# Kernel tuning notes

Hardware: AMD Instinct MI355X
Metric: run time of the kernel (lower is better)

The kernel has to match this reference:

```python
import math
import jax, jax.numpy as jnp
import numpy as np

N, L, H, E, K = 4, 768, 8, 64, 1  # batch, seq (L==S), heads, feat, num_sines


def setup_inputs() -> dict:
    key = jax.random.key(0)
    ks = jax.random.split(key, 8)
    queries = jax.random.normal(ks[0], (N, L, H, E), jnp.float32)
    keys = jax.random.normal(ks[1], (N, L, H, E), jnp.float32)
    values = jax.random.normal(ks[2], (N, L, H, E), jnp.float32)
    attn_mask_add = jnp.zeros((L, L), jnp.float32)
    key_lengths_add = jnp.zeros((N, L), jnp.float32)
    freqs = jax.random.normal(ks[3], (H, E, K), jnp.float32) - 4.0  # init shift
    offsets = jax.random.normal(ks[4], (H, E, K), jnp.float32)
    gains = jax.random.normal(ks[5], (H, E, K), jnp.float32)
    # gains.data /= sqrt(||gains||_{-1}) / 2
    gains = gains / (jnp.sqrt(jnp.linalg.norm(gains, axis=-1, keepdims=True)) / 2.0)
    gate = jax.random.normal(ks[6], (H, E), jnp.float32)
    return dict(queries=queries, keys=keys, values=values,
                attn_mask_add=attn_mask_add, key_lengths_add=key_lengths_add,
                freqs=freqs, offsets=offsets, gains=gains, gate=gate)


def reference(queries, keys, values, attn_mask_add, key_lengths_add,
              freqs, offsets, gains, gate):
    n, l, h, e = queries.shape
    softmax_temp = 1.0 / math.sqrt(e)
    positions = jnp.arange(l, dtype=queries.dtype)  # (L,)
    f = jax.nn.sigmoid(freqs)[None] / 2.0  # (1,H,E,K)
    phases_q = 2.0 * math.pi * f * positions[:, None, None, None] + offsets[None]
    phases_k = 2.0 * math.pi * f * positions[:, None, None, None]
    # interleave cos/sin along last dim -> (L,H,E,2K)
    omega_q = jnp.stack([jnp.cos(phases_q), jnp.sin(phases_q)], axis=-1).reshape(l, h, e, 2 * f.shape[-1])
    omega_k = jnp.stack([jnp.cos(phases_k), jnp.sin(phases_k)], axis=-1).reshape(l, h, e, 2 * f.shape[-1])
    g = jax.nn.softplus(gains)
    g2 = jnp.stack([g, g], axis=-1).reshape(h, e, 2 * f.shape[-1])  # (H,E,2K)
    # positional kernel P: (L,S,H,E)
    P = jnp.einsum('lhdk,hdk,shdk->lshd', omega_q, g2 ** 2, omega_k)
    P = (1.0 - gate) * P + gate  # gated
    QK = jnp.einsum('nlhd,lshd,nshd->nhls', queries, P, keys)
    QK = QK + attn_mask_add[None, None] + key_lengths_add[:, None, None, :]
    A = jax.nn.softmax(softmax_temp * QK, axis=-1)
    V = jnp.einsum('nhls,nshd->nlhd', A, values)
    return V
```

## Files before the change

kernel.cpp:

```cpp
#include <hip/hip_runtime.h>
#include <math.h>
#include <stdint.h>

#define NB 4
#define LQ 768
#define NH 8
#define NE 64
#define ND 192
#define TEMP 0.125f

typedef _Float16 f16;
typedef __attribute__((ext_vector_type(8))) _Float16 f16x8;
typedef __attribute__((ext_vector_type(4))) float f32x4;

__device__ __forceinline__ void stage16(f16* lds_base, const f16* g, int lane) {
#if __has_builtin(__builtin_amdgcn_global_load_lds)
    __builtin_amdgcn_global_load_lds(
        (const __attribute__((address_space(1))) uint32_t*)g,
        (__attribute__((address_space(3))) uint32_t*)lds_base, 16, 0, 0);
#else
    *(uint4*)((char*)lds_base + lane * 16) = *(const uint4*)g;
#endif
}

__global__ __launch_bounds__(256) void sinattn_prepvt(
    const float* __restrict__ Q, const float* __restrict__ K,
    const float* __restrict__ V,
    const float* __restrict__ freqs, const float* __restrict__ offsets,
    const float* __restrict__ gains, const float* __restrict__ gate,
    f16* __restrict__ Qf, f16* __restrict__ Kf, f16* __restrict__ Vt)
{
    if (blockIdx.x < 768) {
        int idx = blockIdx.x * 256 + threadIdx.x;
        int eg = idx & 7, e0 = eg << 3;
        int h  = (idx >> 3) & 7;
        int t  = idx >> 6;
        int l  = t % LQ;
        int n  = t / LQ;
        int nh = (n << 3) | h;
        int he = (h << 6) | e0;

        const float* qp = Q + (size_t)idx * 8;
        const float* kp = K + (size_t)idx * 8;
        float4 q0 = *(const float4*)qp, q1 = *(const float4*)(qp + 4);
        float4 k0 = *(const float4*)kp, k1 = *(const float4*)(kp + 4);
        float qv[8] = {q0.x,q0.y,q0.z,q0.w, q1.x,q1.y,q1.z,q1.w};
        float kv[8] = {k0.x,k0.y,k0.z,k0.w, k1.x,k1.y,k1.z,k1.w};

        float4 fA = *(const float4*)(freqs   + he), fB = *(const float4*)(freqs   + he + 4);
        float4 oA = *(const float4*)(offsets + he), oB = *(const float4*)(offsets + he + 4);
        float4 gA = *(const float4*)(gains   + he), gB = *(const float4*)(gains   + he + 4);
        float4 tA = *(const float4*)(gate    + he), tB = *(const float4*)(gate    + he + 4);
        float fv[8] = {fA.x,fA.y,fA.z,fA.w, fB.x,fB.y,fB.z,fB.w};
        float ov[8] = {oA.x,oA.y,oA.z,oA.w, oB.x,oB.y,oB.z,oB.w};
        float gv[8] = {gA.x,gA.y,gA.z,gA.w, gB.x,gB.y,gB.z,gB.w};
        float tv[8] = {tA.x,tA.y,tA.z,tA.w, tB.x,tB.y,tB.z,tB.w};

        f16x8 oq0, oq1, oq2, ok0, ok1, ok2;
        float lf = (float)l;
        #pragma unroll
        for (int j = 0; j < 8; ++j) {
            float f  = 0.5f / (1.0f + __expf(-fv[j]));
            float gn = gv[j];
            float sp = (gn > 15.0f) ? gn : __logf(1.0f + __expf(gn));
            float gt = tv[j];
            float a  = (1.0f - gt) * sp * sp;
            float fh = __uint_as_float(__float_as_uint(f) & 0xFFFFF000u);
            float fl = f - fh;
            float t0 = lf * fh;
            float tr = t0 - floorf(t0);
            tr = __builtin_fmaf(lf, fl, tr);
            float pk = 6.28318530717958647f * tr;
            float pq = pk + ov[j];
            float sq = __sinf(pq), cq = __cosf(pq);
            float sk = __sinf(pk), ck = __cosf(pk);
            oq0[j] = (f16)(qv[j] * a * cq);
            oq1[j] = (f16)(qv[j] * a * sq);
            oq2[j] = (f16)(qv[j] * gt);
            ok0[j] = (f16)(kv[j] * ck);
            ok1[j] = (f16)(kv[j] * sk);
            ok2[j] = (f16)(kv[j]);
        }
        size_t base = ((size_t)nh * LQ + l) * ND + e0;
        *(f16x8*)(Qf + base)          = oq0;
        *(f16x8*)(Qf + base + NE)     = oq1;
        *(f16x8*)(Qf + base + 2*NE)   = oq2;
        *(f16x8*)(Kf + base)          = ok0;
        *(f16x8*)(Kf + base + NE)     = ok1;
        *(f16x8*)(Kf + base + 2*NE)   = ok2;
    } else {
        __shared__ f16 tile[64][72];
        int b = blockIdx.x - 768;
        int st = b % 12, nh = b / 12;
        int n = nh >> 3, h = nh & 7;
        int s0 = st * 64;
        int tid = threadIdx.x;

        int sl = tid >> 2, e0 = (tid & 3) << 4;
        const float4* vp = (const float4*)(V + ((size_t)(n * LQ + s0 + sl) * NH + h) * NE + e0);
        float4 a0 = vp[0], a1 = vp[1], a2 = vp[2], a3 = vp[3];
        float vv[16] = { a0.x,a0.y,a0.z,a0.w, a1.x,a1.y,a1.z,a1.w,
                         a2.x,a2.y,a2.z,a2.w, a3.x,a3.y,a3.z,a3.w };
        #pragma unroll
        for (int j = 0; j < 16; ++j) tile[e0 + j][sl] = (f16)vv[j];
        __syncthreads();

        int er = tid >> 2, sc = tid & 3;
        f16* op = Vt + ((size_t)nh * NE + er) * LQ + s0 + sc * 16;
        *(uint4*)op       = *(const uint4*)&tile[er][sc * 16];
        *(uint4*)(op + 8) = *(const uint4*)&tile[er][sc * 16 + 8];
    }
}

__global__ __launch_bounds__(256, 2) void sinattn_flash(
    const f16* __restrict__ Qf, const f16* __restrict__ Kf, const f16* __restrict__ Vt,
    const float* __restrict__ mask, const float* __restrict__ keylen,
    float* __restrict__ Op, float* __restrict__ Mp, float* __restrict__ Lp)
{
    __shared__ __attribute__((aligned(16))) f16 sK[2][64 * 24 * 8];
    __shared__ __attribute__((aligned(16))) f16 sV[2][64 * 8 * 8];
    __shared__ __attribute__((aligned(16))) f16 sP[4][16 * 72];

    int tid  = threadIdx.x;
    int wv   = tid >> 6;
    int wvu  = __builtin_amdgcn_readfirstlane(wv);
    int lane = tid & 63;
    int grp  = lane >> 4;
    int r16  = lane & 15;
    int swz  = r16 & 7;

    int bid  = blockIdx.x;
    int nh   = bid & 31;
    int rr2  = bid >> 5;
    int lt   = rr2 >> 1;
    int half = rr2 & 1;
    int n    = nh >> 3;
    int l0   = lt * 64;
    int c0   = half * 6;

    f16x8 qf[6];
    {
        size_t rbase = ((size_t)nh * LQ + l0 + wv * 16 + r16) * ND + grp * 8;
        #pragma unroll
        for (int d0 = 0; d0 < 6; ++d0)
            qf[d0] = *(const f16x8*)(Qf + rbase + d0 * 32);
    }

    int goffK[6], goffV[2];
    #pragma unroll
    for (int i = 0; i < 6; ++i) {
        int p = i * 256 + wv * 64 + lane;
        int r = p / 24, c = p - r * 24;
        int cl = (c & ~7) | ((c & 7) ^ (r & 7));
        goffK[i] = r * ND + cl * 8;
    }
    #pragma unroll
    for (int i = 0; i < 2; ++i) {
        int p = i * 256 + wv * 64 + lane;
        int r = p >> 3, c = p & 7;
        goffV[i] = r * LQ + (c ^ (r & 7)) * 8;
    }
    const f16* Kb = Kf + (size_t)nh * LQ * ND;
    const f16* Vb = Vt + (size_t)nh * NE * LQ;

    {
        const f16* kg = Kb + c0 * 64 * ND;
        const f16* vg = Vb + c0 * 64;
        #pragma unroll
        for (int i = 0; i < 6; ++i)
            stage16(&sK[0][(i * 256 + wvu * 64) * 8], kg + goffK[i], lane);
        #pragma unroll
        for (int i = 0; i < 2; ++i)
            stage16(&sV[0][(i * 256 + wvu * 64) * 8], vg + goffV[i], lane);
    }

    float m_i[4], l_i[4];
    f32x4 O[4];
    #pragma unroll
    for (int rr = 0; rr < 4; ++rr) { m_i[rr] = -INFINITY; l_i[rr] = 0.f; }
    #pragma unroll
    for (int tt = 0; tt < 4; ++tt)
        #pragma unroll
        for (int rr = 0; rr < 4; ++rr) O[tt][rr] = 0.f;

    for (int c = c0; c < c0 + 6; ++c) {
        int cur = c & 1;
        int s0  = c * 64;
        __syncthreads();

        if (c < c0 + 5) {
            const f16* kg = Kb + (s0 + 64) * ND;
            const f16* vg = Vb + (s0 + 64);
            #pragma unroll
            for (int i = 0; i < 6; ++i)
                stage16(&sK[cur ^ 1][(i * 256 + wvu * 64) * 8], kg + goffK[i], lane);
            #pragma unroll
            for (int i = 0; i < 2; ++i)
                stage16(&sV[cur ^ 1][(i * 256 + wvu * 64) * 8], vg + goffV[i], lane);
        }

        float klv[4], mreg[4][4];
        #pragma unroll
        for (int j = 0; j < 4; ++j) klv[j] = keylen[n * LQ + s0 + j * 16 + r16];
        #pragma unroll
        for (int rr = 0; rr < 4; ++rr) {
            int lrow = l0 + wv * 16 + grp * 4 + rr;
            #pragma unroll
            for (int j = 0; j < 4; ++j)
                mreg[rr][j] = mask[lrow * LQ + s0 + j * 16 + r16];
        }

        f32x4 st[4];
        #pragma unroll
        for (int j = 0; j < 4; ++j)
            #pragma unroll
            for (int rr = 0; rr < 4; ++rr) st[j][rr] = 0.f;
        #pragma unroll
        for (int d0 = 0; d0 < 6; ++d0) {
            #pragma unroll
            for (int j = 0; j < 4; ++j) {
                int cc = d0 * 4 + grp;
                int cl = (cc & ~7) | ((cc & 7) ^ swz);
                f16x8 bf = *(const f16x8*)&sK[cur][((j * 16 + r16) * 24 + cl) * 8];
                st[j] = __builtin_amdgcn_mfma_f32_16x16x32_f16(qf[d0], bf, st[j], 0, 0, 0);
            }
        }

        #pragma unroll
        for (int rr = 0; rr < 4; ++rr) {
            float lg[4];
            float mx = -INFINITY;
            #pragma unroll
            for (int j = 0; j < 4; ++j) {
                lg[j] = TEMP * (st[j][rr] + mreg[rr][j] + klv[j]);
                mx = fmaxf(mx, lg[j]);
            }
            #pragma unroll
            for (int d = 1; d < 16; d <<= 1) mx = fmaxf(mx, __shfl_xor(mx, d));
            float mnew  = fmaxf(m_i[rr], mx);
            float alpha = __expf(m_i[rr] - mnew);
            float rs = 0.f;
            #pragma unroll
            for (int j = 0; j < 4; ++j) {
                float p = __expf(lg[j] - mnew);
                rs += p;
                sP[wv][(grp * 4 + rr) * 72 + j * 16 + r16] = (f16)p;
            }
            #pragma unroll
            for (int d = 1; d < 16; d <<= 1) rs += __shfl_xor(rs, d);
            l_i[rr] = l_i[rr] * alpha + rs;
            m_i[rr] = mnew;
            #pragma unroll
            for (int tt = 0; tt < 4; ++tt) O[tt][rr] *= alpha;
        }

        #pragma unroll
        for (int kk = 0; kk < 2; ++kk) {
            f16x8 pa = *(const f16x8*)&sP[wv][r16 * 72 + kk * 32 + grp * 8];
            #pragma unroll
            for (int tt = 0; tt < 4; ++tt) {
                int cc = kk * 4 + grp;
                f16x8 vb = *(const f16x8*)&sV[cur][((tt * 16 + r16) * 8 + (cc ^ swz)) * 8];
                O[tt] = __builtin_amdgcn_mfma_f32_16x16x32_f16(pa, vb, O[tt], 0, 0, 0);
            }
        }
    }

    #pragma unroll
    for (int rr = 0; rr < 4; ++rr) {
        int lrow = l0 + wv * 16 + grp * 4 + rr;
        size_t prow = (size_t)(half * 32 + nh) * LQ + lrow;
        float* op = Op + prow * NE;
        #pragma unroll
        for (int tt = 0; tt < 4; ++tt)
            op[tt * 16 + r16] = O[tt][rr];
        if (r16 == 0) {
            Mp[prow] = m_i[rr];
            Lp[prow] = l_i[rr];
        }
    }
}

__global__ __launch_bounds__(256) void sinattn_merge(
    const float* __restrict__ Op, const float* __restrict__ Mp,
    const float* __restrict__ Lp, float* __restrict__ out)
{
    int idx = blockIdx.x * 256 + threadIdx.x;
    if (idx >= NB * LQ * NH * NE) return;
    int e = idx & 63;
    int h = (idx >> 6) & 7;
    int t = idx >> 9;
    int l = t % LQ;
    int n = t / LQ;
    int nh = (n << 3) | h;
    int row = nh * LQ + l;
    const int HOFF = 32 * LQ;

    float m0 = Mp[row],        m1 = Mp[HOFF + row];
    float l0 = Lp[row],        l1 = Lp[HOFF + row];
    float mm = fmaxf(m0, m1);
    float a0 = __expf(m0 - mm), a1 = __expf(m1 - mm);
    float denom = l0 * a0 + l1 * a1;
    float o0 = Op[(size_t)row * NE + e];
    float o1 = Op[(size_t)(HOFF + row) * NE + e];
    out[idx] = (o0 * a0 + o1 * a1) / denom;
}

extern "C" void kernel_launch(void* const* d_in, const int* in_sizes, int n_in,
                              void* d_out, int out_size, void* d_ws, size_t ws_size,
                              hipStream_t stream)
{
    const float* Q      = (const float*)d_in[0];
    const float* K      = (const float*)d_in[1];
    const float* V      = (const float*)d_in[2];
    const float* mask   = (const float*)d_in[3];
    const float* keylen = (const float*)d_in[4];
    const float* freqs  = (const float*)d_in[5];
    const float* offs   = (const float*)d_in[6];
    const float* gains  = (const float*)d_in[7];
    const float* gate   = (const float*)d_in[8];
    float* out = (float*)d_out;

    const size_t P = (size_t)NB * NH * LQ * ND;
    f16* Qf = (f16*)d_ws;
    f16* Kf = Qf + P;
    f16* Vt = Kf + P;
    float* Op = (float*)(Vt + (size_t)NB * NH * NE * LQ);
    float* Mp = Op + (size_t)2 * 32 * LQ * NE;
    float* Lp = Mp + (size_t)2 * 32 * LQ;

    sinattn_prepvt<<<1152, 256, 0, stream>>>(Q, K, V, freqs, offs, gains, gate,
                                             Qf, Kf, Vt);
    sinattn_flash<<<768, 256, 0, stream>>>(Qf, Kf, Vt, mask, keylen, Op, Mp, Lp);
    sinattn_merge<<<6144, 256, 0, stream>>>(Op, Mp, Lp, out);
}
```

Measured before the change: 122.8 us.

## Drop LDS staging for K/V and give each wave two query row groups

The flash kernel no longer stages K and V tiles in shared memory with double buffering. Each wave now reads K and V fragments directly from global memory into registers and reuses each fragment across two 16-row query groups. The block covers 128 query rows instead of 64, halving the grid to 384 blocks. This removes barriers and LDS traffic but relies on L2/cache for K/V reuse across waves, increases register pressure, and leaves fewer blocks to fill the GPU.

```diff
diff --git a/kernel.cpp b/kernel.cpp
--- a/kernel.cpp
+++ b/kernel.cpp
@@ -12,16 +12,6 @@
 typedef _Float16 f16;
 typedef __attribute__((ext_vector_type(8))) _Float16 f16x8;
 typedef __attribute__((ext_vector_type(4))) float f32x4;
-
-__device__ __forceinline__ void stage16(f16* lds_base, const f16* g, int lane) {
-#if __has_builtin(__builtin_amdgcn_global_load_lds)
-    __builtin_amdgcn_global_load_lds(
-        (const __attribute__((address_space(1))) uint32_t*)g,
-        (__attribute__((address_space(3))) uint32_t*)lds_base, 16, 0, 0);
-#else
-    *(uint4*)((char*)lds_base + lane * 16) = *(const uint4*)g;
-#endif
-}
 
 __global__ __launch_bounds__(256) void sinattn_prepvt(
     const float* __restrict__ Q, const float* __restrict__ K,
@@ -117,166 +107,141 @@
     const float* __restrict__ mask, const float* __restrict__ keylen,
     float* __restrict__ Op, float* __restrict__ Mp, float* __restrict__ Lp)
 {
-    __shared__ __attribute__((aligned(16))) f16 sK[2][64 * 24 * 8];
-    __shared__ __attribute__((aligned(16))) f16 sV[2][64 * 8 * 8];
-    __shared__ __attribute__((aligned(16))) f16 sP[4][16 * 72];
+    __shared__ __attribute__((aligned(16))) f16 sP[4][32 * 72];
 
     int tid  = threadIdx.x;
     int wv   = tid >> 6;
-    int wvu  = __builtin_amdgcn_readfirstlane(wv);
     int lane = tid & 63;
     int grp  = lane >> 4;
     int r16  = lane & 15;
-    int swz  = r16 & 7;
 
     int bid  = blockIdx.x;
     int nh   = bid & 31;
-    int rr2  = bid >> 5;
-    int lt   = rr2 >> 1;
-    int half = rr2 & 1;
+    int rest = bid >> 5;
+    int lt   = rest >> 1;
+    int half = rest & 1;
     int n    = nh >> 3;
-    int l0   = lt * 64;
-    int c0   = half * 6;
-
-    f16x8 qf[6];
-    {
-        size_t rbase = ((size_t)nh * LQ + l0 + wv * 16 + r16) * ND + grp * 8;
-        #pragma unroll
-        for (int d0 = 0; d0 < 6; ++d0)
-            qf[d0] = *(const f16x8*)(Qf + rbase + d0 * 32);
-    }
-
-    int goffK[6], goffV[2];
-    #pragma unroll
-    for (int i = 0; i < 6; ++i) {
-        int p = i * 256 + wv * 64 + lane;
-        int r = p / 24, c = p - r * 24;
-        int cl = (c & ~7) | ((c & 7) ^ (r & 7));
-        goffK[i] = r * ND + cl * 8;
-    }
-    #pragma unroll
-    for (int i = 0; i < 2; ++i) {
-        int p = i * 256 + wv * 64 + lane;
-        int r = p >> 3, c = p & 7;
-        goffV[i] = r * LQ + (c ^ (r & 7)) * 8;
-    }
+    int l0   = lt * 128;
+    int c0   = half * 384;
+
     const f16* Kb = Kf + (size_t)nh * LQ * ND;
     const f16* Vb = Vt + (size_t)nh * NE * LQ;
 
-    {
-        const f16* kg = Kb + c0 * 64 * ND;
-        const f16* vg = Vb + c0 * 64;
-        #pragma unroll
-        for (int i = 0; i < 6; ++i)
-            stage16(&sK[0][(i * 256 + wvu * 64) * 8], kg + goffK[i], lane);
-        #pragma unroll
-        for (int i = 0; i < 2; ++i)
-            stage16(&sV[0][(i * 256 + wvu * 64) * 8], vg + goffV[i], lane);
+    f16x8 qf[2][6];
+    #pragma unroll
+    for (int rg = 0; rg < 2; ++rg) {
+        size_t rbase = ((size_t)nh * LQ + l0 + wv * 32 + rg * 16 + r16) * ND + grp * 8;
+        #pragma unroll
+        for (int d0 = 0; d0 < 6; ++d0)
+            qf[rg][d0] = *(const f16x8*)(Qf + rbase + d0 * 32);
     }
 
-    float m_i[4], l_i[4];
-    f32x4 O[4];
+    float m_i[2][4], l_i[2][4];
+    f32x4 O[2][4];
     #pragma unroll
-    for (int rr = 0; rr < 4; ++rr) { m_i[rr] = -INFINITY; l_i[rr] = 0.f; }
+    for (int rg = 0; rg < 2; ++rg)
+        #pragma unroll
+        for (int rr = 0; rr < 4; ++rr) { m_i[rg][rr] = -INFINITY; l_i[rg][rr] = 0.f; }
     #pragma unroll
-    for (int tt = 0; tt < 4; ++tt)
-        #pragma unroll
-        for (int rr = 0; rr < 4; ++rr) O[tt][rr] = 0.f;
-
-    for (int c = c0; c < c0 + 6; ++c) {
-        int cur = c & 1;
-        int s0  = c * 64;
-        __syncthreads();
-
-        if (c < c0 + 5) {
-            const f16* kg = Kb + (s0 + 64) * ND;
-            const f16* vg = Vb + (s0 + 64);
-            #pragma unroll
-            for (int i = 0; i < 6; ++i)
-                stage16(&sK[cur ^ 1][(i * 256 + wvu * 64) * 8], kg + goffK[i], lane);
-            #pragma unroll
-            for (int i = 0; i < 2; ++i)
-                stage16(&sV[cur ^ 1][(i * 256 + wvu * 64) * 8], vg + goffV[i], lane);
-        }
-
-        float klv[4], mreg[4][4];
+    for (int rg = 0; rg < 2; ++rg)
+        #pragma unroll
+        for (int tt = 0; tt < 4; ++tt)
+            #pragma unroll
+            for (int rr = 0; rr < 4; ++rr) O[rg][tt][rr] = 0.f;
+
+    for (int g = 0; g < 6; ++g) {
+        int s0 = c0 + g * 64;
+
+        f32x4 st[2][4];
+        #pragma unroll
+        for (int rg = 0; rg < 2; ++rg)
+            #pragma unroll
+            for (int j = 0; j < 4; ++j)
+                #pragma unroll
+                for (int rr = 0; rr < 4; ++rr) st[rg][j][rr] = 0.f;
+        #pragma unroll
+        for (int j = 0; j < 4; ++j) {
+            const f16* kp = Kb + (size_t)(s0 + j * 16 + r16) * ND + grp * 8;
+            f16x8 bf[6];
+            #pragma unroll
+            for (int d0 = 0; d0 < 6; ++d0) bf[d0] = *(const f16x8*)(kp + d0 * 32);
+            #pragma unroll
+            for (int d0 = 0; d0 < 6; ++d0) {
+                st[0][j] = __builtin_amdgcn_mfma_f32_16x16x32_f16(qf[0][d0], bf[d0], st[0][j], 0, 0, 0);
+                st[1][j] = __builtin_amdgcn_mfma_f32_16x16x32_f16(qf[1][d0], bf[d0], st[1][j], 0, 0, 0);
+            }
+        }
+
+        f16x8 vb[2][4];
+        #pragma unroll
+        for (int kk = 0; kk < 2; ++kk)
+            #pragma unroll
+            for (int tt = 0; tt < 4; ++tt)
+                vb[kk][tt] = *(const f16x8*)(Vb + (size_t)(tt * 16 + r16) * LQ
+                                             + s0 + kk * 32 + grp * 8);
+
+        float klv[4];
         #pragma unroll
         for (int j = 0; j < 4; ++j) klv[j] = keylen[n * LQ + s0 + j * 16 + r16];
+
+        #pragma unroll
+        for (int rg = 0; rg < 2; ++rg) {
+            #pragma unroll
+            for (int rr = 0; rr < 4; ++rr) {
+                int lrow = l0 + wv * 32 + rg * 16 + grp * 4 + rr;
+                float lg[4];
+                float mx = -INFINITY;
+                #pragma unroll
+                for (int j = 0; j < 4; ++j) {
+                    lg[j] = TEMP * (st[rg][j][rr] + mask[lrow * LQ + s0 + j * 16 + r16] + klv[j]);
+                    mx = fmaxf(mx, lg[j]);
+                }
+                #pragma unroll
+                for (int d = 1; d < 16; d <<= 1) mx = fmaxf(mx, __shfl_xor(mx, d));
+                float mnew  = fmaxf(m_i[rg][rr], mx);
+                float alpha = __expf(m_i[rg][rr] - mnew);
+                float rs = 0.f;
+                #pragma unroll
+                for (int j = 0; j < 4; ++j) {
+                    float p = __expf(lg[j] - mnew);
+                    rs += p;
+                    sP[wv][(rg * 16 + grp * 4 + rr) * 72 + j * 16 + r16] = (f16)p;
+                }
+                #pragma unroll
+                for (int d = 1; d < 16; d <<= 1) rs += __shfl_xor(rs, d);
+                l_i[rg][rr] = l_i[rg][rr] * alpha + rs;
+                m_i[rg][rr] = mnew;
+                #pragma unroll
+                for (int tt = 0; tt < 4; ++tt) O[rg][tt][rr] *= alpha;
+            }
+        }
+
+        #pragma unroll
+        for (int rg = 0; rg < 2; ++rg) {
+            #pragma unroll
+            for (int kk = 0; kk < 2; ++kk) {
+                f16x8 pa = *(const f16x8*)&sP[wv][(rg * 16 + r16) * 72 + kk * 32 + grp * 8];
+                #pragma unroll
+                for (int tt = 0; tt < 4; ++tt)
+                    O[rg][tt] = __builtin_amdgcn_mfma_f32_16x16x32_f16(pa, vb[kk][tt], O[rg][tt], 0, 0, 0);
+            }
+        }
+    }
+
+    #pragma unroll
+    for (int rg = 0; rg < 2; ++rg) {
         #pragma unroll
         for (int rr = 0; rr < 4; ++rr) {
-            int lrow = l0 + wv * 16 + grp * 4 + rr;
-            #pragma unroll
-            for (int j = 0; j < 4; ++j)
-                mreg[rr][j] = mask[lrow * LQ + s0 + j * 16 + r16];
-        }
-
-        f32x4 st[4];
-        #pragma unroll
-        for (int j = 0; j < 4; ++j)
-            #pragma unroll
-            for (int rr = 0; rr < 4; ++rr) st[j][rr] = 0.f;
-        #pragma unroll
-        for (int d0 = 0; d0 < 6; ++d0) {
-            #pragma unroll
-            for (int j = 0; j < 4; ++j) {
-                int cc = d0 * 4 + grp;
-                int cl = (cc & ~7) | ((cc & 7) ^ swz);
-                f16x8 bf = *(const f16x8*)&sK[cur][((j * 16 + r16) * 24 + cl) * 8];
-                st[j] = __builtin_amdgcn_mfma_f32_16x16x32_f16(qf[d0], bf, st[j], 0, 0, 0);
+            int lrow = l0 + wv * 32 + rg * 16 + grp * 4 + rr;
+            size_t prow = (size_t)(half * 32 + nh) * LQ + lrow;
+            float* op = Op + prow * NE;
+            #pragma unroll
+            for (int tt = 0; tt < 4; ++tt)
+                op[tt * 16 + r16] = O[rg][tt][rr];
+            if (r16 == 0) {
+                Mp[prow] = m_i[rg][rr];
+                Lp[prow] = l_i[rg][rr];
             }
-        }
-
-        #pragma unroll
-        for (int rr = 0; rr < 4; ++rr) {
-            float lg[4];
-            float mx = -INFINITY;
-            #pragma unroll
-            for (int j = 0; j < 4; ++j) {
-                lg[j] = TEMP * (st[j][rr] + mreg[rr][j] + klv[j]);
-                mx = fmaxf(mx, lg[j]);
-            }
-            #pragma unroll
-            for (int d = 1; d < 16; d <<= 1) mx = fmaxf(mx, __shfl_xor(mx, d));
-            float mnew  = fmaxf(m_i[rr], mx);
-            float alpha = __expf(m_i[rr] - mnew);
-            float rs = 0.f;
-            #pragma unroll
-            for (int j = 0; j < 4; ++j) {
-                float p = __expf(lg[j] - mnew);
-                rs += p;
-                sP[wv][(grp * 4 + rr) * 72 + j * 16 + r16] = (f16)p;
-            }
-            #pragma unroll
-            for (int d = 1; d < 16; d <<= 1) rs += __shfl_xor(rs, d);
-            l_i[rr] = l_i[rr] * alpha + rs;
-            m_i[rr] = mnew;
-            #pragma unroll
-            for (int tt = 0; tt < 4; ++tt) O[tt][rr] *= alpha;
-        }
-
-        #pragma unroll
-        for (int kk = 0; kk < 2; ++kk) {
-            f16x8 pa = *(const f16x8*)&sP[wv][r16 * 72 + kk * 32 + grp * 8];
-            #pragma unroll
-            for (int tt = 0; tt < 4; ++tt) {
-                int cc = kk * 4 + grp;
-                f16x8 vb = *(const f16x8*)&sV[cur][((tt * 16 + r16) * 8 + (cc ^ swz)) * 8];
-                O[tt] = __builtin_amdgcn_mfma_f32_16x16x32_f16(pa, vb, O[tt], 0, 0, 0);
-            }
-        }
-    }
-
-    #pragma unroll
-    for (int rr = 0; rr < 4; ++rr) {
-        int lrow = l0 + wv * 16 + grp * 4 + rr;
-        size_t prow = (size_t)(half * 32 + nh) * LQ + lrow;
-        float* op = Op + prow * NE;
-        #pragma unroll
-        for (int tt = 0; tt < 4; ++tt)
-            op[tt * 16 + r16] = O[tt][rr];
-        if (r16 == 0) {
-            Mp[prow] = m_i[rr];
-            Lp[prow] = l_i[rr];
         }
     }
 }
@@ -331,6 +296,6 @@
 
     sinattn_prepvt<<<1152, 256, 0, stream>>>(Q, K, V, freqs, offs, gains, gate,
                                              Qf, Kf, Vt);
-    sinattn_flash<<<768, 256, 0, stream>>>(Qf, Kf, Vt, mask, keylen, Op, Mp, Lp);
+    sinattn_flash<<<384, 256, 0, stream>>>(Qf, Kf, Vt, mask, keylen, Op, Mp, Lp);
     sinattn_merge<<<6144, 256, 0, stream>>>(Op, Mp, Lp, out);
 }
```

Result: slower. 145.0 us (+18.1%).

## Single-buffer K in LDS, load V directly to registers, raise occupancy

Applied to the files above, without the earlier changes.

Drops the double-buffered K/V LDS staging in favour of a single K buffer that is refilled after the QK MFMAs, with an extra barrier. V fragments are now read straight from global memory into registers, and mask values are loaded inline. Launch bounds move from 2 to 4 blocks per CU. The aim is to cut LDS footprint and register pressure so more waves can hide latency. The cost is losing the prefetch overlap and doing uncoalesced global V loads on the critical path.

```diff
diff --git a/kernel.cpp b/kernel.cpp
--- a/kernel.cpp
+++ b/kernel.cpp
@@ -112,13 +112,12 @@
     }
 }
 
-__global__ __launch_bounds__(256, 2) void sinattn_flash(
+__global__ __launch_bounds__(256, 4) void sinattn_flash(
     const f16* __restrict__ Qf, const f16* __restrict__ Kf, const f16* __restrict__ Vt,
     const float* __restrict__ mask, const float* __restrict__ keylen,
     float* __restrict__ Op, float* __restrict__ Mp, float* __restrict__ Lp)
 {
-    __shared__ __attribute__((aligned(16))) f16 sK[2][64 * 24 * 8];
-    __shared__ __attribute__((aligned(16))) f16 sV[2][64 * 8 * 8];
+    __shared__ __attribute__((aligned(16))) f16 sK[64 * 24 * 8];
     __shared__ __attribute__((aligned(16))) f16 sP[4][16 * 72];
 
     int tid  = threadIdx.x;
@@ -131,22 +130,17 @@
 
     int bid  = blockIdx.x;
     int nh   = bid & 31;
-    int rr2  = bid >> 5;
-    int lt   = rr2 >> 1;
-    int half = rr2 & 1;
+    int rest = bid >> 5;
+    int lt   = rest >> 1;
+    int half = rest & 1;
     int n    = nh >> 3;
     int l0   = lt * 64;
     int c0   = half * 6;
 
-    f16x8 qf[6];
-    {
-        size_t rbase = ((size_t)nh * LQ + l0 + wv * 16 + r16) * ND + grp * 8;
-        #pragma unroll
-        for (int d0 = 0; d0 < 6; ++d0)
-            qf[d0] = *(const f16x8*)(Qf + rbase + d0 * 32);
-    }
-
-    int goffK[6], goffV[2];
+    const f16* Kb = Kf + (size_t)nh * LQ * ND;
+    const f16* Vb = Vt + (size_t)nh * NE * LQ;
+
+    int goffK[6];
     #pragma unroll
     for (int i = 0; i < 6; ++i) {
         int p = i * 256 + wv * 64 + lane;
@@ -154,24 +148,20 @@
         int cl = (c & ~7) | ((c & 7) ^ (r & 7));
         goffK[i] = r * ND + cl * 8;
     }
-    #pragma unroll
-    for (int i = 0; i < 2; ++i) {
-        int p = i * 256 + wv * 64 + lane;
-        int r = p >> 3, c = p & 7;
-        goffV[i] = r * LQ + (c ^ (r & 7)) * 8;
-    }
-    const f16* Kb = Kf + (size_t)nh * LQ * ND;
-    const f16* Vb = Vt + (size_t)nh * NE * LQ;
 
     {
-        const f16* kg = Kb + c0 * 64 * ND;
-        const f16* vg = Vb + c0 * 64;
+        const f16* kg = Kb + (size_t)c0 * 64 * ND;
         #pragma unroll
         for (int i = 0; i < 6; ++i)
-            stage16(&sK[0][(i * 256 + wvu * 64) * 8], kg + goffK[i], lane);
-        #pragma unroll
-        for (int i = 0; i < 2; ++i)
-            stage16(&sV[0][(i * 256 + wvu * 64) * 8], vg + goffV[i], lane);
+            stage16(&sK[(i * 256 + wvu * 64) * 8], kg + goffK[i], lane);
+    }
+
+    f16x8 qf[6];
+    {
+        size_t rbase = ((size_t)nh * LQ + l0 + wv * 16 + r16) * ND + grp * 8;
+        #pragma unroll
+        for (int d0 = 0; d0 < 6; ++d0)
+            qf[d0] = *(const f16x8*)(Qf + rbase + d0 * 32);
     }
 
     float m_i[4], l_i[4];
@@ -183,32 +173,20 @@
         #pragma unroll
         for (int rr = 0; rr < 4; ++rr) O[tt][rr] = 0.f;
 
-    for (int c = c0; c < c0 + 6; ++c) {
-        int cur = c & 1;
-        int s0  = c * 64;
+    for (int g = 0; g < 6; ++g) {
+        int s0 = (c0 + g) * 64;
         __syncthreads();
 
-        if (c < c0 + 5) {
-            const f16* kg = Kb + (s0 + 64) * ND;
-            const f16* vg = Vb + (s0 + 64);
-            #pragma unroll
-            for (int i = 0; i < 6; ++i)
-                stage16(&sK[cur ^ 1][(i * 256 + wvu * 64) * 8], kg + goffK[i], lane);
-            #pragma unroll
-            for (int i = 0; i < 2; ++i)
-                stage16(&sV[cur ^ 1][(i * 256 + wvu * 64) * 8], vg + goffV[i], lane);
-        }
-
-        float klv[4], mreg[4][4];
+        float klv[4];
         #pragma unroll
         for (int j = 0; j < 4; ++j) klv[j] = keylen[n * LQ + s0 + j * 16 + r16];
-        #pragma unroll
-        for (int rr = 0; rr < 4; ++rr) {
-            int lrow = l0 + wv * 16 + grp * 4 + rr;
-            #pragma unroll
-            for (int j = 0; j < 4; ++j)
-                mreg[rr][j] = mask[lrow * LQ + s0 + j * 16 + r16];
-        }
+        f16x8 vb[2][4];
+        #pragma unroll
+        for (int kk = 0; kk < 2; ++kk)
+            #pragma unroll
+            for (int tt = 0; tt < 4; ++tt)
+                vb[kk][tt] = *(const f16x8*)(Vb + (size_t)(tt * 16 + r16) * LQ
+                                             + s0 + kk * 32 + grp * 8);
 
         f32x4 st[4];
         #pragma unroll
@@ -221,18 +199,28 @@
             for (int j = 0; j < 4; ++j) {
                 int cc = d0 * 4 + grp;
                 int cl = (cc & ~7) | ((cc & 7) ^ swz);
-                f16x8 bf = *(const f16x8*)&sK[cur][((j * 16 + r16) * 24 + cl) * 8];
+                f16x8 bf = *(const f16x8*)&sK[((j * 16 + r16) * 24 + cl) * 8];
                 st[j] = __builtin_amdgcn_mfma_f32_16x16x32_f16(qf[d0], bf, st[j], 0, 0, 0);
             }
         }
 
+        __syncthreads();
+
+        if (g < 5) {
+            const f16* kg = Kb + (size_t)(s0 + 64) * ND;
+            #pragma unroll
+            for (int i = 0; i < 6; ++i)
+                stage16(&sK[(i * 256 + wvu * 64) * 8], kg + goffK[i], lane);
+        }
+
         #pragma unroll
         for (int rr = 0; rr < 4; ++rr) {
+            int lrow = l0 + wv * 16 + grp * 4 + rr;
             float lg[4];
             float mx = -INFINITY;
             #pragma unroll
             for (int j = 0; j < 4; ++j) {
-                lg[j] = TEMP * (st[j][rr] + mreg[rr][j] + klv[j]);
+                lg[j] = TEMP * (st[j][rr] + mask[lrow * LQ + s0 + j * 16 + r16] + klv[j]);
                 mx = fmaxf(mx, lg[j]);
             }
             #pragma unroll
@@ -258,11 +246,8 @@
         for (int kk = 0; kk < 2; ++kk) {
             f16x8 pa = *(const f16x8*)&sP[wv][r16 * 72 + kk * 32 + grp * 8];
             #pragma unroll
-            for (int tt = 0; tt < 4; ++tt) {
-                int cc = kk * 4 + grp;
-                f16x8 vb = *(const f16x8*)&sV[cur][((tt * 16 + r16) * 8 + (cc ^ swz)) * 8];
-                O[tt] = __builtin_amdgcn_mfma_f32_16x16x32_f16(pa, vb, O[tt], 0, 0, 0);
-            }
+            for (int tt = 0; tt < 4; ++tt)
+                O[tt] = __builtin_amdgcn_mfma_f32_16x16x32_f16(pa, vb[kk][tt], O[tt], 0, 0, 0);
         }
     }
 
```

Measured after the change: 176.2 us. 1.44x slower.
